# Kernel tuning notes

Hardware: AMD Instinct MI355X
Metric: run time of the kernel (lower is better)

Reference implementation:

```python
import jax, jax.numpy as jnp
import numpy as np

W_LEN = 8      # window_len
DEPTH = 3      # sig_depth (implementation hardcodes depth-3 truncated signature)


def _seg_exp(d):
    """Truncated tensor-exponential of a linear segment with increment d (N,D)."""
    t1 = d
    t2 = 0.5 * jnp.einsum('ni,nj->nij', d, d)
    t3 = jnp.einsum('nij,nk->nijk', t2, d) / 3.0  # d^{\otimes 3}/6
    return t1, t2, t3


def _signature_depth3(path):
    """path: (N, L, D) -> flattened depth-3 signature (N, D + D^2 + D^3),
    matching signatory.signature ordering (levels concatenated, row-major)."""
    N, L, D = path.shape
    dx = path[:, 1:] - path[:, :-1]          # (N, L-1, D) increments
    s1, s2, s3 = _seg_exp(dx[:, 0])

    def chen_step(carry, d):
        s1, s2, s3 = carry
        t1, t2, t3 = _seg_exp(d)
        n1 = s1 + t1
        n2 = s2 + jnp.einsum('ni,nj->nij', s1, t1) + t2
        n3 = (s3
              + jnp.einsum('nij,nk->nijk', s2, t1)
              + jnp.einsum('ni,njk->nijk', s1, t2)
              + t3)
        return (n1, n2, n3), None

    # scan over the remaining L-2 increments (time axis leading)
    (s1, s2, s3), _ = jax.lax.scan(chen_step, (s1, s2, s3),
                                   jnp.moveaxis(dx[:, 1:], 1, 0))
    return jnp.concatenate([s1, s2.reshape(N, -1), s3.reshape(N, -1)], axis=-1)


def _rolling_windows(x, w_len):
    """x: (B,T,D) -> (B,T,W,D); window t covers [max(0,t-W+1), t],
    left-padded by repeating the first element (clamped indices)."""
    T = x.shape[1]
    idx = jnp.clip(jnp.arange(T)[:, None] - (w_len - 1) + jnp.arange(w_len)[None, :], 0, T - 1)  # (T,W)
    return x[:, idx]  # (B,T,W,D)


def setup_inputs() -> dict:
    key = jax.random.key(0)
    k1, k2, k3 = jax.random.split(key, 3)
    B, T, D = 8, 4096, 8
    sig_channels = D + D * D + D * D * D  # 584
    proj_dim = 128
    x = jax.random.normal(k1, (B, T, D), dtype=jnp.float32)
    w_proj = jax.random.normal(k2, (sig_channels, proj_dim), dtype=jnp.float32) * (1.0 / np.sqrt(sig_channels))
    b_proj = jax.random.normal(k3, (proj_dim,), dtype=jnp.float32) * 0.01
    return {"x": x, "w_proj": w_proj, "b_proj": b_proj}


def reference(x, w_proj, b_proj):
    B, T, D = x.shape
    windows = _rolling_windows(x, W_LEN).reshape(B * T, W_LEN, D)
    sig = _signature_depth3(windows).reshape(B, T, -1)   # (B,T,584)
    return sig @ w_proj + b_proj                          # (B,T,128)
```

## Files before the change

### kernel.cpp

```cpp
#include <hip/hip_runtime.h>
#include <hip/hip_bf16.h>

typedef unsigned short ushort_t;
typedef __attribute__((ext_vector_type(8))) short short8;
typedef __attribute__((ext_vector_type(4))) float floatx4;
typedef __attribute__((ext_vector_type(4))) int intx4;

#define SIG_CH 584
#define KPAD   608
#define NKB    76
#define NPROJ  128
#define ASTRIDE 616
#define TLEN   4096
#define NWIN   32768

__device__ __forceinline__ ushort_t f2bf(float f) {
    unsigned int v; __builtin_memcpy(&v, &f, 4);
    v += 0x7fffu + ((v >> 16) & 1u);
    return (ushort_t)(v >> 16);
}

__global__ void pack_w_kernel(const float* __restrict__ w, ushort_t* __restrict__ wp) {
    int idx = blockIdx.x * 256 + threadIdx.x;
    if (idx >= KPAD * NPROJ) return;
    int n = idx & (NPROJ - 1);
    int c = idx >> 7;
    ushort_t v = 0;
    if (c < SIG_CH) v = f2bf(w[c * NPROJ + n]);
    int kb = c >> 3, kk = c & 7;
    wp[((size_t)kb * NPROJ + n) * 8 + kk] = v;
}

__launch_bounds__(256, 2)
__global__ void sig_gemm_kernel(const float* __restrict__ x,
                                const ushort_t* __restrict__ wp,
                                const float* __restrict__ bias,
                                float* __restrict__ out) {
    __shared__ float    s_dinc[70][8];
    __shared__ ushort_t s_A[64][ASTRIDE];

    const int tid  = threadIdx.x;
    const int blk  = blockIdx.x;
    const int g0   = blk * 64;
    const int b    = g0 >> 12;
    const int t0   = g0 & (TLEN - 1);
    const float* xb = x + (size_t)b * TLEN * 8;

    for (int idx = tid; idx < 70 * 8; idx += 256) {
        int s  = idx >> 3, k = idx & 7;
        int ta = t0 - 7 + s;
        int tb = ta + 1;
        ta = ta < 0 ? 0 : ta;
        tb = tb < 0 ? 0 : tb;
        s_dinc[s][k] = xb[tb * 8 + k] - xb[ta * 8 + k];
    }
    for (int idx = tid; idx < 64 * 32; idx += 256) {
        int r = idx >> 5, c = SIG_CH + (idx & 31);
        s_A[r][c] = 0;
    }
    __syncthreads();

    const int wv   = tid >> 6;
    const int lane = tid & 63;
    const int li   = lane >> 3;
    const int lj   = lane & 7;

    #pragma unroll 1
    for (int ww = 0; ww < 16; ++ww) {
        const int w = wv * 16 + ww;
        float h = 0.f, g = 0.f, s2 = 0.f;
        float s3[8] = {0.f, 0.f, 0.f, 0.f, 0.f, 0.f, 0.f, 0.f};
        #pragma unroll
        for (int st = 0; st < 7; ++st) {
            const floatx4 d0 = *(const floatx4*)(&s_dinc[w + st][0]);
            const floatx4 d1 = *(const floatx4*)(&s_dinc[w + st][4]);
            const float di = s_dinc[w + st][li];
            const float dj = s_dinc[w + st][lj];
            const float c3 = fmaf(dj, fmaf(0.166666667f, di, 0.5f * h), s2);
            s2 = fmaf(dj, fmaf(0.5f, di, h), s2);
            s3[0] = fmaf(c3, d0[0], s3[0]);
            s3[1] = fmaf(c3, d0[1], s3[1]);
            s3[2] = fmaf(c3, d0[2], s3[2]);
            s3[3] = fmaf(c3, d0[3], s3[3]);
            s3[4] = fmaf(c3, d1[0], s3[4]);
            s3[5] = fmaf(c3, d1[1], s3[5]);
            s3[6] = fmaf(c3, d1[2], s3[6]);
            s3[7] = fmaf(c3, d1[3], s3[7]);
            h += di;
            g += dj;
        }
        union { ushort_t u[8]; intx4 v; } pk;
        #pragma unroll
        for (int k = 0; k < 8; ++k) pk.u[k] = f2bf(s3[k]);
        *(intx4*)(&s_A[w][72 + lane * 8]) = pk.v;
        s_A[w][8 + lane] = f2bf(s2);
        if (lane < 8) s_A[w][lane] = f2bf(g);
    }
    __syncthreads();

    const int lrow  = lane & 15;
    const int kgrp  = lane >> 4;
    const int ncol0 = wv * 32 + lrow;

    floatx4 acc[4][2];
    #pragma unroll
    for (int mt = 0; mt < 4; ++mt) {
        acc[mt][0] = floatx4{0.f, 0.f, 0.f, 0.f};
        acc[mt][1] = floatx4{0.f, 0.f, 0.f, 0.f};
    }

    for (int kc = 0; kc < 19; ++kc) {
        const int kb = kc * 4 + kgrp;
        const short8 b0 = *(const short8*)(wp + ((size_t)kb * NPROJ + ncol0) * 8);
        const short8 b1 = *(const short8*)(wp + ((size_t)kb * NPROJ + ncol0 + 16) * 8);
        #pragma unroll
        for (int mt = 0; mt < 4; ++mt) {
            const short8 af = *(const short8*)(&s_A[mt * 16 + lrow][kc * 32 + kgrp * 8]);
            acc[mt][0] = __builtin_amdgcn_mfma_f32_16x16x32_bf16(af, b0, acc[mt][0], 0, 0, 0);
            acc[mt][1] = __builtin_amdgcn_mfma_f32_16x16x32_bf16(af, b1, acc[mt][1], 0, 0, 0);
        }
    }

    const float bias0 = bias[ncol0];
    const float bias1 = bias[ncol0 + 16];
    #pragma unroll
    for (int mt = 0; mt < 4; ++mt) {
        #pragma unroll
        for (int r = 0; r < 4; ++r) {
            const int row = g0 + mt * 16 + kgrp * 4 + r;
            out[(size_t)row * NPROJ + ncol0]      = acc[mt][0][r] + bias0;
            out[(size_t)row * NPROJ + ncol0 + 16] = acc[mt][1][r] + bias1;
        }
    }
}

extern "C" void kernel_launch(void* const* d_in, const int* in_sizes, int n_in,
                              void* d_out, int out_size, void* d_ws, size_t ws_size,
                              hipStream_t stream) {
    const float* x  = (const float*)d_in[0];
    const float* w  = (const float*)d_in[1];
    const float* bp = (const float*)d_in[2];
    ushort_t* wp  = (ushort_t*)d_ws;
    float* out = (float*)d_out;

    hipLaunchKernelGGL(pack_w_kernel, dim3((KPAD * NPROJ + 255) / 256), dim3(256), 0, stream,
                       w, wp);
    hipLaunchKernelGGL(sig_gemm_kernel, dim3(NWIN / 64), dim3(256), 0, stream,
                       x, wp, bp, out);
}
```

Measured before the change: 80.27 us.

## Precompute padded increments in prep kernel and read per-window vectors via scalar loads

The weight-pack kernel now also computes a zero-padded increment array per batch in workspace, so the main kernel no longer subtracts x values or clamps indices when staging increments. Inside the signature loop, the eight wave-uniform increment components are read from global memory at a readfirstlane offset instead of as vector LDS loads, which moves that traffic onto scalar loads. This trades LDS bandwidth for scalar-cache reads and adds a prep-kernel pass that writes about 1 MB of extra data.

Result: no change. 78.72 us (-1.9%).

```diff
diff --git a/kernel.cpp b/kernel.cpp
--- a/kernel.cpp
+++ b/kernel.cpp
@@ -13,6 +13,7 @@
 #define ASTRIDE 616
 #define TLEN   4096
 #define NWIN   32768
+#define DROWS  4103
 
 __device__ __forceinline__ ushort_t f2bf(float f) {
     unsigned int v; __builtin_memcpy(&v, &f, 4);
@@ -20,19 +21,33 @@
     return (ushort_t)(v >> 16);
 }
 
-__global__ void pack_w_kernel(const float* __restrict__ w, ushort_t* __restrict__ wp) {
+__global__ void pack_kernel(const float* __restrict__ w, const float* __restrict__ x,
+                            ushort_t* __restrict__ wp, float* __restrict__ dincP) {
     int idx = blockIdx.x * 256 + threadIdx.x;
-    if (idx >= KPAD * NPROJ) return;
-    int n = idx & (NPROJ - 1);
-    int c = idx >> 7;
-    ushort_t v = 0;
-    if (c < SIG_CH) v = f2bf(w[c * NPROJ + n]);
-    int kb = c >> 3, kk = c & 7;
-    wp[((size_t)kb * NPROJ + n) * 8 + kk] = v;
+    if (idx < KPAD * NPROJ) {
+        int n = idx & (NPROJ - 1);
+        int c = idx >> 7;
+        ushort_t v = 0;
+        if (c < SIG_CH) v = f2bf(w[c * NPROJ + n]);
+        wp[((size_t)(c >> 3) * NPROJ + n) * 8 + (c & 7)] = v;
+        return;
+    }
+    int id2 = idx - KPAD * NPROJ;
+    if (id2 >= 8 * DROWS * 8) return;
+    int k  = id2 & 7;
+    int rr = (id2 >> 3) % DROWS;
+    int b  = (id2 >> 3) / DROWS;
+    float v = 0.f;
+    if (rr >= 8) {
+        int ta = rr - 8;
+        const float* xb = x + (size_t)b * TLEN * 8;
+        v = xb[(ta + 1) * 8 + k] - xb[ta * 8 + k];
+    }
+    dincP[((size_t)b * DROWS + rr) * 8 + k] = v;
 }
 
 __launch_bounds__(256, 2)
-__global__ void sig_gemm_kernel(const float* __restrict__ x,
+__global__ void sig_gemm_kernel(const float* __restrict__ dincP,
                                 const ushort_t* __restrict__ wp,
                                 const float* __restrict__ bias,
                                 float* __restrict__ out) {
@@ -44,15 +59,11 @@
     const int g0   = blk * 64;
     const int b    = g0 >> 12;
     const int t0   = g0 & (TLEN - 1);
-    const float* xb = x + (size_t)b * TLEN * 8;
+    const float* dincB = dincP + (size_t)b * DROWS * 8;
 
     for (int idx = tid; idx < 70 * 8; idx += 256) {
-        int s  = idx >> 3, k = idx & 7;
-        int ta = t0 - 7 + s;
-        int tb = ta + 1;
-        ta = ta < 0 ? 0 : ta;
-        tb = tb < 0 ? 0 : tb;
-        s_dinc[s][k] = xb[tb * 8 + k] - xb[ta * 8 + k];
+        int s = idx >> 3, k = idx & 7;
+        s_dinc[s][k] = dincB[(size_t)(t0 + 1 + s) * 8 + k];
     }
     for (int idx = tid; idx < 64 * 32; idx += 256) {
         int r = idx >> 5, c = SIG_CH + (idx & 31);
@@ -68,24 +79,20 @@
     #pragma unroll 1
     for (int ww = 0; ww < 16; ++ww) {
         const int w = wv * 16 + ww;
+        const int  woff = __builtin_amdgcn_readfirstlane((t0 + 1 + w) * 8);
+        const float* dw = dincB + woff;
+
         float h = 0.f, g = 0.f, s2 = 0.f;
         float s3[8] = {0.f, 0.f, 0.f, 0.f, 0.f, 0.f, 0.f, 0.f};
         #pragma unroll
         for (int st = 0; st < 7; ++st) {
-            const floatx4 d0 = *(const floatx4*)(&s_dinc[w + st][0]);
-            const floatx4 d1 = *(const floatx4*)(&s_dinc[w + st][4]);
             const float di = s_dinc[w + st][li];
             const float dj = s_dinc[w + st][lj];
             const float c3 = fmaf(dj, fmaf(0.166666667f, di, 0.5f * h), s2);
             s2 = fmaf(dj, fmaf(0.5f, di, h), s2);
-            s3[0] = fmaf(c3, d0[0], s3[0]);
-            s3[1] = fmaf(c3, d0[1], s3[1]);
-            s3[2] = fmaf(c3, d0[2], s3[2]);
-            s3[3] = fmaf(c3, d0[3], s3[3]);
-            s3[4] = fmaf(c3, d1[0], s3[4]);
-            s3[5] = fmaf(c3, d1[1], s3[5]);
-            s3[6] = fmaf(c3, d1[2], s3[6]);
-            s3[7] = fmaf(c3, d1[3], s3[7]);
+            #pragma unroll
+            for (int k = 0; k < 8; ++k)
+                s3[k] = fmaf(c3, dw[st * 8 + k], s3[k]);
             h += di;
             g += dj;
         }
@@ -140,11 +147,13 @@
     const float* x  = (const float*)d_in[0];
     const float* w  = (const float*)d_in[1];
     const float* bp = (const float*)d_in[2];
-    ushort_t* wp  = (ushort_t*)d_ws;
+    ushort_t* wp    = (ushort_t*)d_ws;
+    float*    dincP = (float*)((char*)d_ws + 160 * 1024);
     float* out = (float*)d_out;
 
-    hipLaunchKernelGGL(pack_w_kernel, dim3((KPAD * NPROJ + 255) / 256), dim3(256), 0, stream,
-                       w, wp);
+    const int prep_total = KPAD * NPROJ + 8 * DROWS * 8;
+    hipLaunchKernelGGL(pack_kernel, dim3((prep_total + 255) / 256), dim3(256), 0, stream,
+                       w, x, wp, dincP);
     hipLaunchKernelGGL(sig_gemm_kernel, dim3(NWIN / 64), dim3(256), 0, stream,
-                       x, wp, bp, out);
+                       dincP, wp, bp, out);
 }
```
